# Performance work log

Measured on AMD Instinct MI355X. Metric: run time of the kernel, lower is better.

The kernel has to match this reference:

```python
import jax, jax.numpy as jnp
import numpy as np

N = 100000   # nodes
E = 1000000  # edges
F_IN = 128
H = 64
L = 6
C = 10
G = 64       # graphs in batch


def setup_inputs() -> dict:
    key = jax.random.key(0)
    ks = jax.random.split(key, 12)
    x = jax.random.normal(ks[0], (N, F_IN), dtype=jnp.float32)
    edge_index = jax.random.randint(ks[1], (2, E), 0, N, dtype=jnp.int64)
    batch = jnp.sort(jax.random.randint(ks[2], (N,), 0, G, dtype=jnp.int64))
    s = lambda fan: 1.0 / np.sqrt(fan)
    return {
        "x": x,
        "edge_index": edge_index,
        "batch": batch,
        "W0": jax.random.normal(ks[3], (F_IN, H), dtype=jnp.float32) * s(F_IN),
        "b0": jnp.zeros((H,), jnp.float32),
        "Wh": jax.random.normal(ks[4], (L - 1, H, H), dtype=jnp.float32) * s(H),
        "bh": jnp.zeros((L - 1, H), jnp.float32),
        "jkW": jax.random.normal(ks[5], (H * L, H), dtype=jnp.float32) * s(H * L),
        "jkb": jnp.zeros((H,), jnp.float32),
        "W1": jax.random.normal(ks[6], (H, H), dtype=jnp.float32) * s(H),
        "b1": jnp.zeros((H,), jnp.float32),
        "W2": jax.random.normal(ks[7], (H, C), dtype=jnp.float32) * s(H),
        "b2": jnp.zeros((C,), jnp.float32),
    }


def reference(x, edge_index, batch, W0, b0, Wh, bh, jkW, jkb, W1, b1, W2, b2):
    n = x.shape[0]
    # add self-loops (PyG GCNConv default)
    loops = jnp.arange(n, dtype=edge_index.dtype)
    src = jnp.concatenate([edge_index[0], loops])
    dst = jnp.concatenate([edge_index[1], loops])
    # symmetric degree normalization D^{-1/2} (A+I) D^{-1/2}
    deg = jax.ops.segment_sum(jnp.ones_like(dst, x.dtype), dst, num_segments=n)
    disq = jnp.where(deg > 0, deg ** -0.5, 0.0)
    norm = (disq[src] * disq[dst])[:, None]  # [E+N, 1]

    def gcn(h, W, b):
        hW = h @ W                              # [N, H] transform first
        msg = hW[src] * norm                    # gather + normalize
        agg = jax.ops.segment_sum(msg, dst, num_segments=n)  # scatter-add
        return agg + b

    h = jax.nn.relu(gcn(x, W0, b0))
    xs = [h]
    for i in range(L - 1):
        h = jax.nn.relu(gcn(h, Wh[i], bh[i]))
        xs.append(h)
    hcat = jnp.concatenate(xs, axis=-1)         # JK 'cat' -> [N, H*L]
    h = jax.nn.relu(hcat @ jkW + jkb)
    pooled = jax.ops.segment_sum(h, batch, num_segments=G)  # global_add_pool
    h = jax.nn.relu(pooled @ W1 + b1)
    return jax.nn.softmax(h @ W2 + b2, axis=-1)  # [G, C]
```

## Files before the change

kernel.cpp:

```cpp
#include <hip/hip_runtime.h>
#include <hip/hip_fp16.h>

#define NN 100000
#define NE 1000000
#define F_INF 128
#define HID 64
#define NLAY 6
#define NCLS 10
#define NGRAPH 64
#define PART_SZ 12500
#define SCAT_BLKS (((NE + 2047) / 2048) * 8)
#define GEMM_GRID ((NN + 63) / 64)

__device__ __forceinline__ float4 h4f(ushort4 u) {
    __half2 lo = *reinterpret_cast<__half2*>(&u);
    __half2 hi = *reinterpret_cast<__half2*>(reinterpret_cast<unsigned short*>(&u) + 2);
    float2 a = __half22float2(lo);
    float2 b = __half22float2(hi);
    return make_float4(a.x, a.y, b.x, b.y);
}

__device__ __forceinline__ ushort4 f4h(float4 v) {
    __half2 lo = __floats2half2_rn(v.x, v.y);
    __half2 hi = __floats2half2_rn(v.z, v.w);
    ushort4 u;
    *reinterpret_cast<__half2*>(&u) = lo;
    *reinterpret_cast<__half2*>(reinterpret_cast<unsigned short*>(&u) + 2) = hi;
    return u;
}

__global__ void k_hist(const int* __restrict__ dst, int* __restrict__ counts, int e) {
    int i0 = blockIdx.x * 1024 + threadIdx.x;
    #pragma unroll
    for (int k = 0; k < 4; k++) {
        int i = i0 + k * 256;
        if (i < e) atomicAdd(&counts[dst[i]], 1);
    }
}

__global__ void k_blocksum(const int* __restrict__ counts, int* __restrict__ bsum, int n) {
    int i = blockIdx.x * 256 + threadIdx.x;
    int v = (i < n) ? counts[i] : 0;
    #pragma unroll
    for (int off = 32; off >= 1; off >>= 1) v += __shfl_down(v, off);
    __shared__ int ws[4];
    if ((threadIdx.x & 63) == 0) ws[threadIdx.x >> 6] = v;
    __syncthreads();
    if (threadIdx.x == 0) bsum[blockIdx.x] = ws[0] + ws[1] + ws[2] + ws[3];
}

__global__ void k_scanbsum(int* __restrict__ bsum, int nb) {
    __shared__ int sh[512];
    int t = threadIdx.x;
    int v = (t < nb) ? bsum[t] : 0;
    sh[t] = v; __syncthreads();
    for (int off = 1; off < 512; off <<= 1) {
        int x = (t >= off) ? sh[t - off] : 0;
        __syncthreads();
        sh[t] += x; __syncthreads();
    }
    if (t < nb) bsum[t] = sh[t] - v;
}

__global__ void k_scanwrite(const int* __restrict__ counts, const int* __restrict__ bsumx,
                            int* __restrict__ rowptr, int* __restrict__ wptr,
                            float* __restrict__ disq, int n, int e) {
    __shared__ int sh[256];
    int t = threadIdx.x;
    int i = blockIdx.x * 256 + t;
    int v = (i < n) ? counts[i] : 0;
    sh[t] = v; __syncthreads();
    for (int off = 1; off < 256; off <<= 1) {
        int x = (t >= off) ? sh[t - off] : 0;
        __syncthreads();
        sh[t] += x; __syncthreads();
    }
    int excl = sh[t] - v + bsumx[blockIdx.x];
    if (i < n) {
        rowptr[i] = excl;
        wptr[i]   = excl;
        disq[i]   = rsqrtf((float)(v + 1));
    }
    if (i == 0) rowptr[n] = e;
}

__global__ __launch_bounds__(256) void k_scatter_gemm0(
    const int* __restrict__ src, const int* __restrict__ dst,
    int* __restrict__ wptr, int* __restrict__ csr, int e,
    const float* __restrict__ x, const float* __restrict__ W0,
    const float* __restrict__ disq, unsigned short* __restrict__ C16, int n)
{
    __shared__ float Ws[32 * 64];
    __shared__ float As[64 * 36];

    if (blockIdx.x < SCAT_BLKS) {
        int part = blockIdx.x & 7;
        int i0 = (blockIdx.x >> 3) * 2048 + threadIdx.x;
        #pragma unroll
        for (int k = 0; k < 8; k++) {
            int i = i0 + k * 256;
            if (i < e) {
                int d = dst[i];
                if (d / PART_SZ == part) {
                    int pos = atomicAdd(&wptr[d], 1);
                    csr[pos] = src[i];
                }
            }
        }
        return;
    }

    const int tid  = threadIdx.x;
    const int col4 = (tid & 15) * 4;
    const int rowq = tid >> 4;
    const int base = (blockIdx.x - SCAT_BLKS) * 64;
    const int ar   = tid >> 3;
    const int ac4  = (tid & 7) * 4;

    float4 wreg[2], areg[2];
    #pragma unroll
    for (int i = 0; i < 2; i++)
        wreg[i] = *(const float4*)(W0 + (size_t)(i * 256 + tid) * 4);
    #pragma unroll
    for (int rr = 0; rr < 2; rr++) {
        int row = base + ar + rr * 32;
        areg[rr] = make_float4(0.f, 0.f, 0.f, 0.f);
        if (row < n) areg[rr] = *(const float4*)(x + (size_t)row * F_INF + ac4);
    }
    #pragma unroll
    for (int i = 0; i < 2; i++)
        *(float4*)(Ws + (size_t)(i * 256 + tid) * 4) = wreg[i];
    #pragma unroll
    for (int rr = 0; rr < 2; rr++)
        *(float4*)(As + (size_t)(ar + rr * 32) * 36 + ac4) = areg[rr];
    __syncthreads();

    float4 acc[4];
    #pragma unroll
    for (int r = 0; r < 4; r++) acc[r] = make_float4(0.f, 0.f, 0.f, 0.f);

    for (int k0 = 0; k0 < F_INF; k0 += 32) {
        const bool more = (k0 + 32) < F_INF;
        if (more) {
            #pragma unroll
            for (int i = 0; i < 2; i++)
                wreg[i] = *(const float4*)(W0 + (size_t)(k0 + 32) * 64 + (i * 256 + tid) * 4);
            #pragma unroll
            for (int rr = 0; rr < 2; rr++) {
                int row = base + ar + rr * 32;
                areg[rr] = make_float4(0.f, 0.f, 0.f, 0.f);
                if (row < n) areg[rr] = *(const float4*)(x + (size_t)row * F_INF + k0 + 32 + ac4);
            }
        }
        #pragma unroll 8
        for (int k = 0; k < 32; k++) {
            float4 w = *(const float4*)(Ws + k * 64 + col4);
            float a0 = As[(rowq * 4 + 0) * 36 + k];
            float a1 = As[(rowq * 4 + 1) * 36 + k];
            float a2 = As[(rowq * 4 + 2) * 36 + k];
            float a3 = As[(rowq * 4 + 3) * 36 + k];
            acc[0].x = fmaf(a0, w.x, acc[0].x); acc[0].y = fmaf(a0, w.y, acc[0].y);
            acc[0].z = fmaf(a0, w.z, acc[0].z); acc[0].w = fmaf(a0, w.w, acc[0].w);
            acc[1].x = fmaf(a1, w.x, acc[1].x); acc[1].y = fmaf(a1, w.y, acc[1].y);
            acc[1].z = fmaf(a1, w.z, acc[1].z); acc[1].w = fmaf(a1, w.w, acc[1].w);
            acc[2].x = fmaf(a2, w.x, acc[2].x); acc[2].y = fmaf(a2, w.y, acc[2].y);
            acc[2].z = fmaf(a2, w.z, acc[2].z); acc[2].w = fmaf(a2, w.w, acc[2].w);
            acc[3].x = fmaf(a3, w.x, acc[3].x); acc[3].y = fmaf(a3, w.y, acc[3].y);
            acc[3].z = fmaf(a3, w.z, acc[3].z); acc[3].w = fmaf(a3, w.w, acc[3].w);
        }
        __syncthreads();
        if (more) {
            #pragma unroll
            for (int i = 0; i < 2; i++)
                *(float4*)(Ws + (size_t)(i * 256 + tid) * 4) = wreg[i];
            #pragma unroll
            for (int rr = 0; rr < 2; rr++)
                *(float4*)(As + (size_t)(ar + rr * 32) * 36 + ac4) = areg[rr];
            __syncthreads();
        }
    }

    #pragma unroll
    for (int r = 0; r < 4; r++) {
        int row = base + rowq * 4 + r;
        if (row < n) {
            float s = disq[row];
            float4 o;
            o.x = acc[r].x * s; o.y = acc[r].y * s;
            o.z = acc[r].z * s; o.w = acc[r].w * s;
            ((ushort4*)C16)[(size_t)row * 16 + (tid & 15)] = f4h(o);
        }
    }
}

__global__ __launch_bounds__(256) void k_gemm_dual(
    const unsigned short* __restrict__ A16,
    const float* __restrict__ W,
    const float* __restrict__ jkw,
    const float* __restrict__ disq,
    unsigned short* __restrict__ C16,
    unsigned short* __restrict__ jkacc16,
    int jk_mode, int n)
{
    __shared__ float Ws[64 * 64];
    __shared__ float Ws2[64 * 64];
    __shared__ float As[64 * 68];
    const int tid  = threadIdx.x;
    const int col4 = (tid & 15) * 4;
    const int rowq = tid >> 4;
    const int base = blockIdx.x * 64;

    #pragma unroll
    for (int i = 0; i < 4; i++) {
        float4 v = *(const float4*)(W + (size_t)(i * 256 + tid) * 4);
        *(float4*)(Ws + (size_t)(i * 256 + tid) * 4) = v;
        float4 v2 = *(const float4*)(jkw + (size_t)(i * 256 + tid) * 4);
        *(float4*)(Ws2 + (size_t)(i * 256 + tid) * 4) = v2;
    }
    {
        const ushort4* Ah = (const ushort4*)A16;
        #pragma unroll
        for (int rr = 0; rr < 4; rr++) {
            int row = base + rowq + rr * 16;
            float4 v = make_float4(0.f, 0.f, 0.f, 0.f);
            if (row < n) v = h4f(Ah[(size_t)row * 16 + (tid & 15)]);
            *(float4*)(As + (size_t)(rowq + rr * 16) * 68 + col4) = v;
        }
    }
    __syncthreads();

    float4 acc[4], acc2[4];
    #pragma unroll
    for (int r = 0; r < 4; r++) {
        acc[r]  = make_float4(0.f, 0.f, 0.f, 0.f);
        acc2[r] = make_float4(0.f, 0.f, 0.f, 0.f);
    }

    #pragma unroll 4
    for (int k = 0; k < 64; k++) {
        float4 w  = *(const float4*)(Ws  + k * 64 + col4);
        float4 w2 = *(const float4*)(Ws2 + k * 64 + col4);
        float a0 = As[(rowq * 4 + 0) * 68 + k];
        float a1 = As[(rowq * 4 + 1) * 68 + k];
        float a2 = As[(rowq * 4 + 2) * 68 + k];
        float a3 = As[(rowq * 4 + 3) * 68 + k];
        acc[0].x = fmaf(a0, w.x, acc[0].x); acc[0].y = fmaf(a0, w.y, acc[0].y);
        acc[0].z = fmaf(a0, w.z, acc[0].z); acc[0].w = fmaf(a0, w.w, acc[0].w);
        acc[1].x = fmaf(a1, w.x, acc[1].x); acc[1].y = fmaf(a1, w.y, acc[1].y);
        acc[1].z = fmaf(a1, w.z, acc[1].z); acc[1].w = fmaf(a1, w.w, acc[1].w);
        acc[2].x = fmaf(a2, w.x, acc[2].x); acc[2].y = fmaf(a2, w.y, acc[2].y);
        acc[2].z = fmaf(a2, w.z, acc[2].z); acc[2].w = fmaf(a2, w.w, acc[2].w);
        acc[3].x = fmaf(a3, w.x, acc[3].x); acc[3].y = fmaf(a3, w.y, acc[3].y);
        acc[3].z = fmaf(a3, w.z, acc[3].z); acc[3].w = fmaf(a3, w.w, acc[3].w);
        acc2[0].x = fmaf(a0, w2.x, acc2[0].x); acc2[0].y = fmaf(a0, w2.y, acc2[0].y);
        acc2[0].z = fmaf(a0, w2.z, acc2[0].z); acc2[0].w = fmaf(a0, w2.w, acc2[0].w);
        acc2[1].x = fmaf(a1, w2.x, acc2[1].x); acc2[1].y = fmaf(a1, w2.y, acc2[1].y);
        acc2[1].z = fmaf(a1, w2.z, acc2[1].z); acc2[1].w = fmaf(a1, w2.w, acc2[1].w);
        acc2[2].x = fmaf(a2, w2.x, acc2[2].x); acc2[2].y = fmaf(a2, w2.y, acc2[2].y);
        acc2[2].z = fmaf(a2, w2.z, acc2[2].z); acc2[2].w = fmaf(a2, w2.w, acc2[2].w);
        acc2[3].x = fmaf(a3, w2.x, acc2[3].x); acc2[3].y = fmaf(a3, w2.y, acc2[3].y);
        acc2[3].z = fmaf(a3, w2.z, acc2[3].z); acc2[3].w = fmaf(a3, w2.w, acc2[3].w);
    }

    #pragma unroll
    for (int r = 0; r < 4; r++) {
        int row = base + rowq * 4 + r;
        if (row < n) {
            float s = disq[row];
            float4 o;
            o.x = acc[r].x * s; o.y = acc[r].y * s;
            o.z = acc[r].z * s; o.w = acc[r].w * s;
            ((ushort4*)C16)[(size_t)row * 16 + (tid & 15)] = f4h(o);
            if (jk_mode == 1) {
                ((ushort4*)jkacc16)[(size_t)row * 16 + (tid & 15)] = f4h(acc2[r]);
            } else {
                float4 p = h4f(((const ushort4*)jkacc16)[(size_t)row * 16 + (tid & 15)]);
                p.x += acc2[r].x; p.y += acc2[r].y;
                p.z += acc2[r].z; p.w += acc2[r].w;
                ((ushort4*)jkacc16)[(size_t)row * 16 + (tid & 15)] = f4h(p);
            }
        }
    }
}

__global__ __launch_bounds__(256) void k_gather(
    const int* __restrict__ rowptr, const int* __restrict__ csr,
    const unsigned short* __restrict__ hW16, const float* __restrict__ disq,
    const float* __restrict__ bias, unsigned short* __restrict__ hout16, int n)
{
    const ushort4* hW4 = (const ushort4*)hW16;
    int wid  = (blockIdx.x * 256 + threadIdx.x) >> 6;
    if (wid >= n) return;
    int lane = threadIdx.x & 63;
    int fb = lane & 15;
    int es = lane >> 4;
    int j  = rowptr[wid];
    int r1 = rowptr[wid + 1];
    float4 v  = make_float4(0.f, 0.f, 0.f, 0.f);
    float4 v2 = make_float4(0.f, 0.f, 0.f, 0.f);
    if (es == 0) v = h4f(hW4[(size_t)wid * 16 + fb]);
    while (j < r1) {
        int cnt = min(r1 - j, 64);
        int idx = (lane < cnt) ? csr[j + lane] : 0;
        for (int jj = 0; jj < cnt; jj += 16) {
            int i0 = jj + es, i1 = jj + 4 + es, i2 = jj + 8 + es, i3 = jj + 12 + es;
            int s0 = __shfl(idx, i0 & 63);
            int s1 = __shfl(idx, i1 & 63);
            int s2 = __shfl(idx, i2 & 63);
            int s3 = __shfl(idx, i3 & 63);
            float4 t0 = h4f(hW4[(size_t)s0 * 16 + fb]);
            float4 t1 = h4f(hW4[(size_t)s1 * 16 + fb]);
            float4 t2 = h4f(hW4[(size_t)s2 * 16 + fb]);
            float4 t3 = h4f(hW4[(size_t)s3 * 16 + fb]);
            if (i0 < cnt) { v.x  += t0.x; v.y  += t0.y; v.z  += t0.z; v.w  += t0.w; }
            if (i1 < cnt) { v2.x += t1.x; v2.y += t1.y; v2.z += t1.z; v2.w += t1.w; }
            if (i2 < cnt) { v.x  += t2.x; v.y  += t2.y; v.z  += t2.z; v.w  += t2.w; }
            if (i3 < cnt) { v2.x += t3.x; v2.y += t3.y; v2.z += t3.z; v2.w += t3.w; }
        }
        j += cnt;
    }
    v.x += v2.x; v.y += v2.y; v.z += v2.z; v.w += v2.w;
    v.x += __shfl_xor(v.x, 16); v.y += __shfl_xor(v.y, 16);
    v.z += __shfl_xor(v.z, 16); v.w += __shfl_xor(v.w, 16);
    v.x += __shfl_xor(v.x, 32); v.y += __shfl_xor(v.y, 32);
    v.z += __shfl_xor(v.z, 32); v.w += __shfl_xor(v.w, 32);
    if (es == 0) {
        float s = disq[wid];
        float4 b = ((const float4*)bias)[fb];
        float4 o;
        o.x = fmaxf(fmaf(s, v.x, b.x), 0.f);
        o.y = fmaxf(fmaf(s, v.y, b.y), 0.f);
        o.z = fmaxf(fmaf(s, v.z, b.z), 0.f);
        o.w = fmaxf(fmaf(s, v.w, b.w), 0.f);
        ((ushort4*)hout16)[(size_t)wid * 16 + fb] = f4h(o);
    }
}

__global__ __launch_bounds__(256) void k_jkfin_pool(
    const unsigned short* __restrict__ A16,
    const float* __restrict__ W,
    const unsigned short* __restrict__ jkacc16,
    const float* __restrict__ bias,
    const int* __restrict__ batch,
    float* __restrict__ pooled,
    int n)
{
    __shared__ float Ws[64 * 64];
    __shared__ float As[64 * 68];
    const int tid  = threadIdx.x;
    const int col4 = (tid & 15) * 4;
    const int rowq = tid >> 4;
    const int base = blockIdx.x * 64;

    #pragma unroll
    for (int i = 0; i < 4; i++) {
        float4 v = *(const float4*)(W + (size_t)(i * 256 + tid) * 4);
        *(float4*)(Ws + (size_t)(i * 256 + tid) * 4) = v;
    }
    {
        const ushort4* Ah = (const ushort4*)A16;
        #pragma unroll
        for (int rr = 0; rr < 4; rr++) {
            int row = base + rowq + rr * 16;
            float4 v = make_float4(0.f, 0.f, 0.f, 0.f);
            if (row < n) v = h4f(Ah[(size_t)row * 16 + (tid & 15)]);
            *(float4*)(As + (size_t)(rowq + rr * 16) * 68 + col4) = v;
        }
    }
    __syncthreads();

    float4 acc[4];
    #pragma unroll
    for (int r = 0; r < 4; r++) acc[r] = make_float4(0.f, 0.f, 0.f, 0.f);
    #pragma unroll 8
    for (int k = 0; k < 64; k++) {
        float4 w = *(const float4*)(Ws + k * 64 + col4);
        float a0 = As[(rowq * 4 + 0) * 68 + k];
        float a1 = As[(rowq * 4 + 1) * 68 + k];
        float a2 = As[(rowq * 4 + 2) * 68 + k];
        float a3 = As[(rowq * 4 + 3) * 68 + k];
        acc[0].x = fmaf(a0, w.x, acc[0].x); acc[0].y = fmaf(a0, w.y, acc[0].y);
        acc[0].z = fmaf(a0, w.z, acc[0].z); acc[0].w = fmaf(a0, w.w, acc[0].w);
        acc[1].x = fmaf(a1, w.x, acc[1].x); acc[1].y = fmaf(a1, w.y, acc[1].y);
        acc[1].z = fmaf(a1, w.z, acc[1].z); acc[1].w = fmaf(a1, w.w, acc[1].w);
        acc[2].x = fmaf(a2, w.x, acc[2].x); acc[2].y = fmaf(a2, w.y, acc[2].y);
        acc[2].z = fmaf(a2, w.z, acc[2].z); acc[2].w = fmaf(a2, w.w, acc[2].w);
        acc[3].x = fmaf(a3, w.x, acc[3].x); acc[3].y = fmaf(a3, w.y, acc[3].y);
        acc[3].z = fmaf(a3, w.z, acc[3].z); acc[3].w = fmaf(a3, w.w, acc[3].w);
    }
    __syncthreads();

    float* slab = Ws;
    #pragma unroll
    for (int i = tid; i < 4096; i += 256) slab[i] = 0.f;
    __syncthreads();

    float4 bb = *(const float4*)(bias + col4);
    int curg = -1;
    float4 s4 = make_float4(0.f, 0.f, 0.f, 0.f);
    #pragma unroll
    for (int r = 0; r < 4; r++) {
        int row = base + rowq * 4 + r;
        if (row < n) {
            float4 p = h4f(((const ushort4*)jkacc16)[(size_t)row * 16 + (tid & 15)]);
            float4 vv;
            vv.x = fmaxf(acc[r].x + p.x + bb.x, 0.f);
            vv.y = fmaxf(acc[r].y + p.y + bb.y, 0.f);
            vv.z = fmaxf(acc[r].z + p.z + bb.z, 0.f);
            vv.w = fmaxf(acc[r].w + p.w + bb.w, 0.f);
            int g = batch[row];
            if (g != curg) {
                if (curg >= 0) {
                    atomicAdd(&slab[curg * 64 + col4 + 0], s4.x);
                    atomicAdd(&slab[curg * 64 + col4 + 1], s4.y);
                    atomicAdd(&slab[curg * 64 + col4 + 2], s4.z);
                    atomicAdd(&slab[curg * 64 + col4 + 3], s4.w);
                }
                curg = g; s4 = vv;
            } else {
                s4.x += vv.x; s4.y += vv.y; s4.z += vv.z; s4.w += vv.w;
            }
        }
    }
    if (curg >= 0) {
        atomicAdd(&slab[curg * 64 + col4 + 0], s4.x);
        atomicAdd(&slab[curg * 64 + col4 + 1], s4.y);
        atomicAdd(&slab[curg * 64 + col4 + 2], s4.z);
        atomicAdd(&slab[curg * 64 + col4 + 3], s4.w);
    }
    __syncthreads();

    int g0 = batch[base];
    int g1 = batch[(base + 63 < n) ? (base + 63) : (n - 1)];
    int cnt = (g1 - g0 + 1) * 64;
    for (int i = tid; i < cnt; i += 256) {
        int g = g0 + (i >> 6);
        int c = i & 63;
        float v = slab[g * 64 + c];
        if (v != 0.f) atomicAdd(&pooled[g * 64 + c], v);
    }
}

__global__ __launch_bounds__(64) void k_head(
    const float* __restrict__ pooled,
    const float* __restrict__ W1, const float* __restrict__ b1,
    const float* __restrict__ W2, const float* __restrict__ b2,
    float* __restrict__ out)
{
    __shared__ float p[64];
    __shared__ float h1[64];
    __shared__ float lg[16];
    const int g = blockIdx.x;
    const int t = threadIdx.x;

    p[t] = pooled[g * 64 + t];
    __syncthreads();

    float acc = b1[t];
    #pragma unroll 8
    for (int k = 0; k < 64; k++) acc = fmaf(p[k], W1[k * 64 + t], acc);
    h1[t] = fmaxf(acc, 0.f);
    __syncthreads();

    if (t < NCLS) {
        float a = b2[t];
        #pragma unroll 8
        for (int j = 0; j < 64; j++) a = fmaf(h1[j], W2[j * NCLS + t], a);
        lg[t] = a;
    }
    __syncthreads();

    if (t == 0) {
        float mx = lg[0];
        #pragma unroll
        for (int c = 1; c < NCLS; c++) mx = fmaxf(mx, lg[c]);
        float ssum = 0.f;
        float e[NCLS];
        #pragma unroll
        for (int c = 0; c < NCLS; c++) { e[c] = __expf(lg[c] - mx); ssum += e[c]; }
        float inv = 1.0f / ssum;
        #pragma unroll
        for (int c = 0; c < NCLS; c++) out[g * NCLS + c] = e[c] * inv;
    }
}

extern "C" void kernel_launch(void* const* d_in, const int* in_sizes, int n_in,
                              void* d_out, int out_size, void* d_ws, size_t ws_size,
                              hipStream_t stream) {
    (void)in_sizes; (void)n_in; (void)out_size; (void)ws_size;
    const float* x     = (const float*)d_in[0];
    const int*   ei    = (const int*)d_in[1];
    const int*   batch = (const int*)d_in[2];
    const float* W0    = (const float*)d_in[3];
    const float* b0    = (const float*)d_in[4];
    const float* Wh    = (const float*)d_in[5];
    const float* bh    = (const float*)d_in[6];
    const float* jkW   = (const float*)d_in[7];
    const float* jkb   = (const float*)d_in[8];
    const float* W1    = (const float*)d_in[9];
    const float* b1    = (const float*)d_in[10];
    const float* W2    = (const float*)d_in[11];
    const float* b2    = (const float*)d_in[12];

    const int* src = ei;
    const int* dst = ei + NE;

    float*          fws     = (float*)d_ws;
    float*          disq    = fws;
    unsigned short* hWb     = (unsigned short*)(disq + 100352);
    unsigned short* h16     = hWb + (size_t)NN * 64;
    unsigned short* jkacc16 = h16 + (size_t)NN * 64;
    float*          pooled  = (float*)(jkacc16 + (size_t)NN * 64);
    int*            counts  = (int*)(pooled + 4096);
    int*            rowptr  = counts + 100352;
    int*            wptr    = rowptr + 100352;
    int*            bsum    = wptr + 100352;
    int*            csr     = bsum + 512;

    const int NB_N = (NN + 255) / 256;

    hipMemsetAsync(counts, 0, (size_t)NN * sizeof(int), stream);
    k_hist<<<(NE + 1023) / 1024, 256, 0, stream>>>(dst, counts, NE);
    k_blocksum<<<NB_N, 256, 0, stream>>>(counts, bsum, NN);
    k_scanbsum<<<1, 512, 0, stream>>>(bsum, NB_N);
    k_scanwrite<<<NB_N, 256, 0, stream>>>(counts, bsum, rowptr, wptr, disq, NN, NE);

    k_scatter_gemm0<<<SCAT_BLKS + GEMM_GRID, 256, 0, stream>>>(
        src, dst, wptr, csr, NE, x, W0, disq, hWb, NN);

    const int gather_grid = (NN + 3) / 4;
    k_gather<<<gather_grid, 256, 0, stream>>>(rowptr, csr, hWb, disq, b0, h16, NN);
    for (int l = 1; l < NLAY; l++) {
        const float* W   = Wh + (size_t)(l - 1) * 64 * 64;
        const float* jw  = jkW + (size_t)(l - 1) * 64 * 64;
        int          jkm = (l == 1) ? 1 : 2;
        k_gemm_dual<<<GEMM_GRID, 256, 0, stream>>>(h16, W, jw, disq, hWb, jkacc16, jkm, NN);
        k_gather<<<gather_grid, 256, 0, stream>>>(rowptr, csr, hWb, disq,
                                                  bh + (size_t)(l - 1) * 64, h16, NN);
    }

    hipMemsetAsync(pooled, 0, 64 * 64 * sizeof(float), stream);
    k_jkfin_pool<<<GEMM_GRID, 256, 0, stream>>>(h16, jkW + (size_t)5 * 64 * 64, jkacc16,
                                                jkb, batch, pooled, NN);
    k_head<<<NGRAPH, 64, 0, stream>>>(pooled, W1, b1, W2, b2, (float*)d_out);
}
```

Baseline: 514.0 us.

## Fuse per-layer GEMM and JK accumulation into the gather kernel

Drops the separate dual-GEMM kernel. Each wavefront that aggregates a node's neighbours now applies the next layer's weight matrix and its JK weight slice straight away, using wavefront shuffles and reading weights from global memory. Ping-pong hW buffers are added so a layer reads one buffer while writing the other. This removes the h16 round-trip through memory and five kernel launches. In exchange, each thread re-reads the weights per node from global/L1 instead of shared memory, and the matmul runs as 64-lane shuffles rather than a tiled GEMM.

```diff
diff --git a/kernel.cpp b/kernel.cpp
--- a/kernel.cpp
+++ b/kernel.cpp
@@ -27,6 +27,16 @@
     *reinterpret_cast<__half2*>(&u) = lo;
     *reinterpret_cast<__half2*>(reinterpret_cast<unsigned short*>(&u) + 2) = hi;
     return u;
+}
+
+__device__ __forceinline__ unsigned short f2h(float v) {
+    __half h = __float2half_rn(v);
+    return *reinterpret_cast<unsigned short*>(&h);
+}
+
+__device__ __forceinline__ float h2f(unsigned short u) {
+    __half h = *reinterpret_cast<__half*>(&u);
+    return __half2float(h);
 }
 
 __global__ void k_hist(const int* __restrict__ dst, int* __restrict__ counts, int e) {
@@ -193,93 +203,86 @@
     }
 }
 
-__global__ __launch_bounds__(256) void k_gemm_dual(
-    const unsigned short* __restrict__ A16,
-    const float* __restrict__ W,
+__global__ __launch_bounds__(256) void k_gather_fused(
+    const int* __restrict__ rowptr, const int* __restrict__ csr,
+    const unsigned short* __restrict__ hW16in, const float* __restrict__ disq,
+    const float* __restrict__ bias,
+    const float* __restrict__ Wn,
     const float* __restrict__ jkw,
-    const float* __restrict__ disq,
-    unsigned short* __restrict__ C16,
+    unsigned short* __restrict__ hW16out,
     unsigned short* __restrict__ jkacc16,
     int jk_mode, int n)
 {
-    __shared__ float Ws[64 * 64];
-    __shared__ float Ws2[64 * 64];
-    __shared__ float As[64 * 68];
-    const int tid  = threadIdx.x;
-    const int col4 = (tid & 15) * 4;
-    const int rowq = tid >> 4;
-    const int base = blockIdx.x * 64;
-
-    #pragma unroll
-    for (int i = 0; i < 4; i++) {
-        float4 v = *(const float4*)(W + (size_t)(i * 256 + tid) * 4);
-        *(float4*)(Ws + (size_t)(i * 256 + tid) * 4) = v;
-        float4 v2 = *(const float4*)(jkw + (size_t)(i * 256 + tid) * 4);
-        *(float4*)(Ws2 + (size_t)(i * 256 + tid) * 4) = v2;
-    }
-    {
-        const ushort4* Ah = (const ushort4*)A16;
-        #pragma unroll
-        for (int rr = 0; rr < 4; rr++) {
-            int row = base + rowq + rr * 16;
-            float4 v = make_float4(0.f, 0.f, 0.f, 0.f);
-            if (row < n) v = h4f(Ah[(size_t)row * 16 + (tid & 15)]);
-            *(float4*)(As + (size_t)(rowq + rr * 16) * 68 + col4) = v;
-        }
-    }
-    __syncthreads();
-
-    float4 acc[4], acc2[4];
-    #pragma unroll
-    for (int r = 0; r < 4; r++) {
-        acc[r]  = make_float4(0.f, 0.f, 0.f, 0.f);
-        acc2[r] = make_float4(0.f, 0.f, 0.f, 0.f);
-    }
-
-    #pragma unroll 4
-    for (int k = 0; k < 64; k++) {
-        float4 w  = *(const float4*)(Ws  + k * 64 + col4);
-        float4 w2 = *(const float4*)(Ws2 + k * 64 + col4);
-        float a0 = As[(rowq * 4 + 0) * 68 + k];
-        float a1 = As[(rowq * 4 + 1) * 68 + k];
-        float a2 = As[(rowq * 4 + 2) * 68 + k];
-        float a3 = As[(rowq * 4 + 3) * 68 + k];
-        acc[0].x = fmaf(a0, w.x, acc[0].x); acc[0].y = fmaf(a0, w.y, acc[0].y);
-        acc[0].z = fmaf(a0, w.z, acc[0].z); acc[0].w = fmaf(a0, w.w, acc[0].w);
-        acc[1].x = fmaf(a1, w.x, acc[1].x); acc[1].y = fmaf(a1, w.y, acc[1].y);
-        acc[1].z = fmaf(a1, w.z, acc[1].z); acc[1].w = fmaf(a1, w.w, acc[1].w);
-        acc[2].x = fmaf(a2, w.x, acc[2].x); acc[2].y = fmaf(a2, w.y, acc[2].y);
-        acc[2].z = fmaf(a2, w.z, acc[2].z); acc[2].w = fmaf(a2, w.w, acc[2].w);
-        acc[3].x = fmaf(a3, w.x, acc[3].x); acc[3].y = fmaf(a3, w.y, acc[3].y);
-        acc[3].z = fmaf(a3, w.z, acc[3].z); acc[3].w = fmaf(a3, w.w, acc[3].w);
-        acc2[0].x = fmaf(a0, w2.x, acc2[0].x); acc2[0].y = fmaf(a0, w2.y, acc2[0].y);
-        acc2[0].z = fmaf(a0, w2.z, acc2[0].z); acc2[0].w = fmaf(a0, w2.w, acc2[0].w);
-        acc2[1].x = fmaf(a1, w2.x, acc2[1].x); acc2[1].y = fmaf(a1, w2.y, acc2[1].y);
-        acc2[1].z = fmaf(a1, w2.z, acc2[1].z); acc2[1].w = fmaf(a1, w2.w, acc2[1].w);
-        acc2[2].x = fmaf(a2, w2.x, acc2[2].x); acc2[2].y = fmaf(a2, w2.y, acc2[2].y);
-        acc2[2].z = fmaf(a2, w2.z, acc2[2].z); acc2[2].w = fmaf(a2, w2.w, acc2[2].w);
-        acc2[3].x = fmaf(a3, w2.x, acc2[3].x); acc2[3].y = fmaf(a3, w2.y, acc2[3].y);
-        acc2[3].z = fmaf(a3, w2.z, acc2[3].z); acc2[3].w = fmaf(a3, w2.w, acc2[3].w);
-    }
-
-    #pragma unroll
-    for (int r = 0; r < 4; r++) {
-        int row = base + rowq * 4 + r;
-        if (row < n) {
-            float s = disq[row];
-            float4 o;
-            o.x = acc[r].x * s; o.y = acc[r].y * s;
-            o.z = acc[r].z * s; o.w = acc[r].w * s;
-            ((ushort4*)C16)[(size_t)row * 16 + (tid & 15)] = f4h(o);
-            if (jk_mode == 1) {
-                ((ushort4*)jkacc16)[(size_t)row * 16 + (tid & 15)] = f4h(acc2[r]);
-            } else {
-                float4 p = h4f(((const ushort4*)jkacc16)[(size_t)row * 16 + (tid & 15)]);
-                p.x += acc2[r].x; p.y += acc2[r].y;
-                p.z += acc2[r].z; p.w += acc2[r].w;
-                ((ushort4*)jkacc16)[(size_t)row * 16 + (tid & 15)] = f4h(p);
-            }
-        }
+    const ushort4* hW4 = (const ushort4*)hW16in;
+    int wid  = (blockIdx.x * 256 + threadIdx.x) >> 6;
+    if (wid >= n) return;
+    int lane = threadIdx.x & 63;
+    int fb = lane & 15;
+    int es = lane >> 4;
+    int j  = rowptr[wid];
+    int r1 = rowptr[wid + 1];
+    float4 v  = make_float4(0.f, 0.f, 0.f, 0.f);
+    float4 v2 = make_float4(0.f, 0.f, 0.f, 0.f);
+    if (es == 0) v = h4f(hW4[(size_t)wid * 16 + fb]);
+    while (j < r1) {
+        int cnt = min(r1 - j, 64);
+        int idx = (lane < cnt) ? csr[j + lane] : 0;
+        for (int jj = 0; jj < cnt; jj += 16) {
+            int i0 = jj + es, i1 = jj + 4 + es, i2 = jj + 8 + es, i3 = jj + 12 + es;
+            int s0 = __shfl(idx, i0 & 63);
+            int s1 = __shfl(idx, i1 & 63);
+            int s2 = __shfl(idx, i2 & 63);
+            int s3 = __shfl(idx, i3 & 63);
+            float4 t0 = h4f(hW4[(size_t)s0 * 16 + fb]);
+            float4 t1 = h4f(hW4[(size_t)s1 * 16 + fb]);
+            float4 t2 = h4f(hW4[(size_t)s2 * 16 + fb]);
+            float4 t3 = h4f(hW4[(size_t)s3 * 16 + fb]);
+            if (i0 < cnt) { v.x  += t0.x; v.y  += t0.y; v.z  += t0.z; v.w  += t0.w; }
+            if (i1 < cnt) { v2.x += t1.x; v2.y += t1.y; v2.z += t1.z; v2.w += t1.w; }
+            if (i2 < cnt) { v.x  += t2.x; v.y  += t2.y; v.z  += t2.z; v.w  += t2.w; }
+            if (i3 < cnt) { v2.x += t3.x; v2.y += t3.y; v2.z += t3.z; v2.w += t3.w; }
+        }
+        j += cnt;
+    }
+    v.x += v2.x; v.y += v2.y; v.z += v2.z; v.w += v2.w;
+    v.x += __shfl_xor(v.x, 16); v.y += __shfl_xor(v.y, 16);
+    v.z += __shfl_xor(v.z, 16); v.w += __shfl_xor(v.w, 16);
+    v.x += __shfl_xor(v.x, 32); v.y += __shfl_xor(v.y, 32);
+    v.z += __shfl_xor(v.z, 32); v.w += __shfl_xor(v.w, 32);
+
+    float s = disq[wid];
+    float4 b = ((const float4*)bias)[fb];
+    float4 h;
+    h.x = fmaxf(fmaf(s, v.x, b.x), 0.f);
+    h.y = fmaxf(fmaf(s, v.y, b.y), 0.f);
+    h.z = fmaxf(fmaf(s, v.z, b.z), 0.f);
+    h.w = fmaxf(fmaf(s, v.w, b.w), 0.f);
+
+    float accw = 0.f, accj = 0.f;
+    #pragma unroll
+    for (int c = 0; c < 16; c++) {
+        float h0 = __shfl(h.x, c);
+        float h1 = __shfl(h.y, c);
+        float h2 = __shfl(h.z, c);
+        float h3 = __shfl(h.w, c);
+        const float* wp = Wn  + (size_t)c * 256 + lane;
+        const float* jp = jkw + (size_t)c * 256 + lane;
+        accw = fmaf(h0, wp[0],   accw);
+        accw = fmaf(h1, wp[64],  accw);
+        accw = fmaf(h2, wp[128], accw);
+        accw = fmaf(h3, wp[192], accw);
+        accj = fmaf(h0, jp[0],   accj);
+        accj = fmaf(h1, jp[64],  accj);
+        accj = fmaf(h2, jp[128], accj);
+        accj = fmaf(h3, jp[192], accj);
+    }
+
+    size_t oidx = (size_t)wid * 64 + lane;
+    hW16out[oidx] = f2h(accw * s);
+    if (jk_mode == 1) {
+        jkacc16[oidx] = f2h(accj);
+    } else {
+        jkacc16[oidx] = f2h(h2f(jkacc16[oidx]) + accj);
     }
 }
 
@@ -507,8 +510,9 @@
 
     float*          fws     = (float*)d_ws;
     float*          disq    = fws;
-    unsigned short* hWb     = (unsigned short*)(disq + 100352);
-    unsigned short* h16     = hWb + (size_t)NN * 64;
+    unsigned short* hWbA    = (unsigned short*)(disq + 100352);
+    unsigned short* hWbB    = hWbA + (size_t)NN * 64;
+    unsigned short* h16     = hWbB + (size_t)NN * 64;
     unsigned short* jkacc16 = h16 + (size_t)NN * 64;
     float*          pooled  = (float*)(jkacc16 + (size_t)NN * 64);
     int*            counts  = (int*)(pooled + 4096);
@@ -526,18 +530,21 @@
     k_scanwrite<<<NB_N, 256, 0, stream>>>(counts, bsum, rowptr, wptr, disq, NN, NE);
 
     k_scatter_gemm0<<<SCAT_BLKS + GEMM_GRID, 256, 0, stream>>>(
-        src, dst, wptr, csr, NE, x, W0, disq, hWb, NN);
+        src, dst, wptr, csr, NE, x, W0, disq, hWbA, NN);
 
     const int gather_grid = (NN + 3) / 4;
-    k_gather<<<gather_grid, 256, 0, stream>>>(rowptr, csr, hWb, disq, b0, h16, NN);
-    for (int l = 1; l < NLAY; l++) {
-        const float* W   = Wh + (size_t)(l - 1) * 64 * 64;
-        const float* jw  = jkW + (size_t)(l - 1) * 64 * 64;
-        int          jkm = (l == 1) ? 1 : 2;
-        k_gemm_dual<<<GEMM_GRID, 256, 0, stream>>>(h16, W, jw, disq, hWb, jkacc16, jkm, NN);
-        k_gather<<<gather_grid, 256, 0, stream>>>(rowptr, csr, hWb, disq,
-                                                  bh + (size_t)(l - 1) * 64, h16, NN);
-    }
+    unsigned short* bufs[2] = { hWbA, hWbB };
+    for (int l = 0; l < 5; l++) {
+        const float* gb  = (l == 0) ? b0 : (bh + (size_t)(l - 1) * 64);
+        const float* Wn  = Wh + (size_t)l * 64 * 64;
+        const float* jw  = jkW + (size_t)l * 64 * 64;
+        int          jkm = (l == 0) ? 1 : 2;
+        k_gather_fused<<<gather_grid, 256, 0, stream>>>(
+            rowptr, csr, bufs[l & 1], disq, gb, Wn, jw,
+            bufs[(l + 1) & 1], jkacc16, jkm, NN);
+    }
+    k_gather<<<gather_grid, 256, 0, stream>>>(rowptr, csr, bufs[1], disq,
+                                              bh + (size_t)4 * 64, h16, NN);
 
     hipMemsetAsync(pooled, 0, 64 * 64 * sizeof(float), stream);
     k_jkfin_pool<<<GEMM_GRID, 256, 0, stream>>>(h16, jkW + (size_t)5 * 64 * 64, jkacc16,
```

Result: slower. 778.7 us (+51.5%).
